# Kernel tuning notes

Measured on AMD Instinct MI355X. Metric: run time of the kernel, lower is better.

Reference implementation:

```python
import jax, jax.numpy as jnp
import numpy as np
from jax import lax

IN_C, OUT_C = 256, 128
HID = (IN_C // 8) // 2   # hidden_channels = 16
NL = 9                   # num_layer
SHIFTS = (1, 5)
DN = ('NCHW', 'OIHW', 'NCHW')

def _base_kernels():
    d1 = np.zeros((4, 1, 3, 3), np.float32)
    d1[0, 0, 0, 0] = -1.0
    d1[1, 0, 0, 1] = -1.0
    d1[2, 0, 0, 2] = -1.0
    d1[3, 0, 1, 2] = -1.0
    d2 = d1[:, :, ::-1, ::-1].copy()
    return np.concatenate([d1, d2], 0)  # (8,1,3,3)

# each of the 8 fixed shift kernels tiled per channel -> (8, HID, 1, 3, 3)
_KER = jnp.asarray(np.tile(_base_kernels()[:, None], (1, HID, 1, 1, 1)))

def _branch(cen, in_w, in_b, w1, w2, w3, sc, shift):
    # input projection conv (kernel 1 or 3, 'same' padding)
    h = lax.conv_general_dilated(cen, in_w, (1, 1), 'SAME', dimension_numbers=DN)
    h = h + in_b[None, :, None, None]
    # 8 fixed dilated depthwise 3x3 convs
    deltas = [lax.conv_general_dilated(h, _KER[k], (1, 1), 'SAME',
                                       rhs_dilation=(shift, shift),
                                       feature_group_count=HID,
                                       dimension_numbers=DN)
              for k in range(8)]
    x = jnp.concatenate(deltas + [h], 1)  # (b, NL*HID, H, W)
    b, c, H, W = x.shape
    xg = x.reshape(b, NL, HID, H, W)
    # grouped 1x1 convs (groups=NL) == per-group 16x16 matmuls
    o1 = jnp.einsum('gdc,bgchw->bgdhw', w1, xg)
    o2 = jnp.einsum('gdc,bgchw->bgdhw', w2, xg)
    o3 = jnp.einsum('gdc,bgchw->bgdhw', w3, xg)
    # logits[b,p,q,h,w] = sc * sum_c o2[b,p,c]*o1[b,q,c]  (torch sums dim=3 of out1*out2*scale)
    logits = sc * jnp.einsum('bpchw,bqchw->bpqhw', o2, o1)
    attn = jax.nn.softmax(logits, axis=2)  # softmax over q (torch dim=2)
    out = jnp.einsum('bpqhw,bqchw->bpchw', attn, o3)
    return out.reshape(b, NL * HID, H, W)

def setup_inputs():
    key = jax.random.key(0)
    ks = jax.random.split(key, 16)
    B, H, W = 4, 192, 192
    s = 0.05
    return {
        'cen': jax.random.normal(ks[0], (B, IN_C, H, W), jnp.float32),
        'in_w0': jax.random.normal(ks[1], (HID, IN_C, 1, 1), jnp.float32) * s,
        'in_b0': jax.random.normal(ks[2], (HID,), jnp.float32) * s,
        'in_w1': jax.random.normal(ks[3], (HID, IN_C, 3, 3), jnp.float32) * s,
        'in_b1': jax.random.normal(ks[4], (HID,), jnp.float32) * s,
        'w1_0': jax.random.normal(ks[5], (NL, HID, HID), jnp.float32) * s,
        'w2_0': jax.random.normal(ks[6], (NL, HID, HID), jnp.float32) * s,
        'w3_0': jax.random.normal(ks[7], (NL, HID, HID), jnp.float32) * s,
        'w1_1': jax.random.normal(ks[8], (NL, HID, HID), jnp.float32) * s,
        'w2_1': jax.random.normal(ks[9], (NL, HID, HID), jnp.float32) * s,
        'w3_1': jax.random.normal(ks[10], (NL, HID, HID), jnp.float32) * s,
        'scale': jax.random.normal(ks[11], (len(SHIFTS),), jnp.float32) * s,
        'out_w': jax.random.normal(ks[12], (OUT_C, NL * HID * len(SHIFTS), 1, 1), jnp.float32) * s,
        'out_b': jax.random.normal(ks[13], (OUT_C,), jnp.float32) * s,
    }

def reference(cen, in_w0, in_b0, in_w1, in_b1, w1_0, w2_0, w3_0,
              w1_1, w2_1, w3_1, scale, out_w, out_b):
    o0 = _branch(cen, in_w0, in_b0, w1_0, w2_0, w3_0, scale[0], SHIFTS[0])
    o1 = _branch(cen, in_w1, in_b1, w1_1, w2_1, w3_1, scale[1], SHIFTS[1])
    cat = jnp.concatenate([o0, o1], 1)  # (b, 288, H, W)
    return jnp.einsum('oi,bihw->bohw', out_w[:, :, 0, 0], cat) + out_b[None, :, None, None]
```

## Files before the change

### kernel.cpp

```cpp
#include <hip/hip_runtime.h>
#include <hip/hip_bf16.h>
#include <cstddef>
#include <cstdint>

#define BATCH 4
#define INC   256
#define HID   16
#define NL    9
#define HH    192
#define WW    192
#define PIX   (HH*WW)
#define BPIX  (BATCH*PIX)
#define OUTC  128
#define CATC  (NL*HID*2)
#define CATK  160

typedef __attribute__((ext_vector_type(8))) short bf16x8;
typedef __attribute__((ext_vector_type(4))) float f32x4;
typedef unsigned short ushort_t;

__device__ inline unsigned short f2bf(float f) {
  unsigned int u = __float_as_uint(f);
  u += 0x7FFF + ((u >> 16) & 1);
  return (unsigned short)(u >> 16);
}
__device__ inline float bf2f(unsigned short s) {
  return __uint_as_float(((unsigned)s) << 16);
}
__device__ inline unsigned pack2(float a, float b) {
  return (unsigned)f2bf(a) | ((unsigned)f2bf(b) << 16);
}
__device__ inline bf16x8 cvt8(float4 a, float4 b) {
  union { bf16x8 v; unsigned u[4]; } r;
  r.u[0] = pack2(a.x, a.y); r.u[1] = pack2(a.z, a.w);
  r.u[2] = pack2(b.x, b.y); r.u[3] = pack2(b.z, b.w);
  return r.v;
}

__global__ __launch_bounds__(256) void kernelP(const float* __restrict__ cen,
                                               ushort_t* __restrict__ th,
                                               ushort_t* __restrict__ tl) {
  __shared__ float t[256][17];
  const int b = blockIdx.z, y = blockIdx.y, x0 = blockIdx.x * 16;
  const int tid = threadIdx.x;
#pragma unroll
  for (int k = 0; k < 16; ++k) {
    int i = tid + k * 256; int c = i >> 4, xl = i & 15;
    t[c][xl] = cen[((size_t)(b * 256 + c)) * PIX + (size_t)y * WW + x0 + xl];
  }
  __syncthreads();
  const size_t obase = (((size_t)b * HH + y) * WW + x0) * 256;
#pragma unroll
  for (int xl = 0; xl < 16; ++xl) {
    float v = t[tid][xl];
    unsigned short hi = f2bf(v);
    th[obase + (size_t)xl * 256 + tid] = hi;
    tl[obase + (size_t)xl * 256 + tid] = f2bf(v - bf2f(hi));
  }
}

__global__ __launch_bounds__(256) void wprepA(
    const float* __restrict__ w0, const float* __restrict__ w1,
    ushort_t* __restrict__ wA0hi, ushort_t* __restrict__ wA0lo,
    ushort_t* __restrict__ wA1hi, ushort_t* __restrict__ wA1lo) {
  int idx = blockIdx.x * 256 + threadIdx.x;
  if (idx < 36864) {
    int j = idx & 7, l = (idx >> 3) & 63, kc = (idx >> 9) & 7, s = idx >> 12;
    int d = l & 15, c = kc * 32 + (l >> 4) * 8 + j;
    float v = w1[(size_t)(d * 256 + c) * 9 + s];
    unsigned short hi = f2bf(v);
    wA1hi[idx] = hi; wA1lo[idx] = f2bf(v - bf2f(hi));
  }
  if (idx < 4096) {
    int j = idx & 7, l = (idx >> 3) & 63, kc = idx >> 9;
    int d = l & 15, c = kc * 32 + (l >> 4) * 8 + j;
    float v = w0[d * 256 + c];
    unsigned short hi = f2bf(v);
    wA0hi[idx] = hi; wA0lo[idx] = f2bf(v - bf2f(hi));
  }
}

__global__ __launch_bounds__(256) void wprepB(const float* __restrict__ out_w,
                                              ushort_t* __restrict__ wb) {
  int idx = blockIdx.x * 256 + threadIdx.x;
  if (idx >= 2 * OUTC * CATK) return;
  int k = idx % CATK; int rest = idx / CATK;
  int o = rest % OUTC; int br = rest / OUTC;
  float v = (k < 144) ? out_w[o * CATC + br * 144 + k] : 0.f;
  wb[idx] = f2bf(v);
}

__global__ __launch_bounds__(256) void wprepM(
    const float* __restrict__ w1_0, const float* __restrict__ w2_0,
    const float* __restrict__ w3_0, const float* __restrict__ w1_1,
    const float* __restrict__ w2_1, const float* __restrict__ w3_1,
    ushort_t* __restrict__ wm) {
  int idx = blockIdx.x * 256 + threadIdx.x;
  if (idx >= 2 * 27 * 512) return;
  int j = idx & 7;
  int lane = (idx >> 3) & 63;
  int blk = idx >> 9;
  int g = blk % 9, mat = (blk / 9) % 3, br = blk / 27;
  int d = lane & 15, k = (lane >> 4) * 8 + j;
  float v = 0.f;
  if (k < 16) {
    const float* w;
    if (br == 0) w = (mat == 0) ? w1_0 : (mat == 1) ? w2_0 : w3_0;
    else         w = (mat == 0) ? w1_1 : (mat == 1) ? w2_1 : w3_1;
    v = w[(g * 16 + d) * 16 + k];
    if (g < 8) v = -v;
  }
  wm[idx] = f2bf(v);
}

template <bool SAFE>
__device__ inline void a_tile(const ushort_t* __restrict__ th,
                              const ushort_t* __restrict__ tl,
                              const ushort_t* __restrict__ wA0hi,
                              const ushort_t* __restrict__ wA0lo,
                              const ushort_t* __restrict__ wA1hi,
                              const ushort_t* __restrict__ wA1lo,
                              int b, int y, int px, f32x4& acc0, f32x4& acc1) {
  const int lane = threadIdx.x & 63;
  const int quad = lane >> 4;
  const bf16x8 bz = {0, 0, 0, 0, 0, 0, 0, 0};
#pragma unroll
  for (int sy = 0; sy < 3; ++sy) {
    const int yy = y + sy - 1;
    const bool yok = SAFE || ((unsigned)yy < (unsigned)HH);
#pragma unroll
    for (int sx = 0; sx < 3; ++sx) {
      const int xx = px + sx - 1;
      const bool ok = SAFE || (yok && ((unsigned)xx < (unsigned)WW));
      const int cy = SAFE ? yy : (ok ? yy : 0);
      const int cx = SAFE ? xx : (ok ? xx : 0);
      const size_t base = (((size_t)(b * HH + cy) * WW) + cx) * 256 + quad * 8;
      const int s = sy * 3 + sx;
      const ushort_t* wh = wA1hi + s * 4096 + lane * 8;
      const ushort_t* wl = wA1lo + s * 4096 + lane * 8;
#pragma unroll
      for (int kc = 0; kc < 8; ++kc) {
        bf16x8 bhi = *(const bf16x8*)(th + base + kc * 32);
        bf16x8 blo = *(const bf16x8*)(tl + base + kc * 32);
        if (!SAFE && !ok) { bhi = bz; blo = bz; }
        bf16x8 ahi = *(const bf16x8*)(wh + kc * 512);
        bf16x8 alo = *(const bf16x8*)(wl + kc * 512);
        acc1 = __builtin_amdgcn_mfma_f32_16x16x32_bf16(ahi, bhi, acc1, 0, 0, 0);
        acc1 = __builtin_amdgcn_mfma_f32_16x16x32_bf16(ahi, blo, acc1, 0, 0, 0);
        acc1 = __builtin_amdgcn_mfma_f32_16x16x32_bf16(alo, bhi, acc1, 0, 0, 0);
        if (s == 4) {
          bf16x8 a0h = *(const bf16x8*)(wA0hi + kc * 512 + lane * 8);
          bf16x8 a0l = *(const bf16x8*)(wA0lo + kc * 512 + lane * 8);
          acc0 = __builtin_amdgcn_mfma_f32_16x16x32_bf16(a0h, bhi, acc0, 0, 0, 0);
          acc0 = __builtin_amdgcn_mfma_f32_16x16x32_bf16(a0h, blo, acc0, 0, 0, 0);
          acc0 = __builtin_amdgcn_mfma_f32_16x16x32_bf16(a0l, bhi, acc0, 0, 0, 0);
        }
      }
    }
  }
}

__global__ __launch_bounds__(256) void kernelA_mfma(
    const ushort_t* __restrict__ th, const ushort_t* __restrict__ tl,
    const ushort_t* __restrict__ wA0hi, const ushort_t* __restrict__ wA0lo,
    const ushort_t* __restrict__ wA1hi, const ushort_t* __restrict__ wA1lo,
    const float* __restrict__ b0, const float* __restrict__ b1,
    float* __restrict__ h0, float* __restrict__ h1) {
  const int lane = threadIdx.x & 63, wave = threadIdx.x >> 6;
  const int n = lane & 15, quad = lane >> 4;
  const int y = blockIdx.y, b = blockIdx.z;
  const int wpx0 = blockIdx.x * 64 + wave * 16;
  const int px = wpx0 + n;
  f32x4 acc0 = {0.f, 0.f, 0.f, 0.f}, acc1 = {0.f, 0.f, 0.f, 0.f};

  const bool safe = (y >= 1) && (y <= HH - 2) && (wpx0 >= 1) && (wpx0 + 16 <= WW - 1);
  if (safe)
    a_tile<true>(th, tl, wA0hi, wA0lo, wA1hi, wA1lo, b, y, px, acc0, acc1);
  else
    a_tile<false>(th, tl, wA0hi, wA0lo, wA1hi, wA1lo, b, y, px, acc0, acc1);

  const size_t pb = ((size_t)b * PIX + (size_t)y * WW + px) * 16 + quad * 4;
  float4 r0, r1;
  r0.x = acc0[0] + b0[quad * 4 + 0]; r0.y = acc0[1] + b0[quad * 4 + 1];
  r0.z = acc0[2] + b0[quad * 4 + 2]; r0.w = acc0[3] + b0[quad * 4 + 3];
  r1.x = acc1[0] + b1[quad * 4 + 0]; r1.y = acc1[1] + b1[quad * 4 + 1];
  r1.z = acc1[2] + b1[quad * 4 + 2]; r1.w = acc1[3] + b1[quad * 4 + 3];
  *(float4*)(h0 + pb) = r0;
  *(float4*)(h1 + pb) = r1;
}

__global__ __launch_bounds__(256) void kernelA_f32(
    const float* __restrict__ cen, const float* __restrict__ w0,
    const float* __restrict__ b0,  const float* __restrict__ w1,
    const float* __restrict__ b1,  float* __restrict__ h0,
    float* __restrict__ h1) {
  __shared__ float lds[16 * 18 * 18];
  const int lx = threadIdx.x, ly = threadIdx.y;
  const int tid = ly * 16 + lx;
  const int x0 = blockIdx.x * 16, y0 = blockIdx.y * 16, b = blockIdx.z;

  float acc0[16], acc1[16];
#pragma unroll
  for (int d = 0; d < 16; ++d) { acc0[d] = 0.f; acc1[d] = 0.f; }

  for (int cb = 0; cb < INC; cb += 16) {
    __syncthreads();
    for (int i = tid; i < 16 * 18 * 18; i += 256) {
      int c = i / 324; int rem = i - c * 324;
      int yy = rem / 18; int xx = rem - yy * 18;
      int gy = y0 + yy - 1, gx = x0 + xx - 1;
      float v = 0.f;
      if (gy >= 0 && gy < HH && gx >= 0 && gx < WW)
        v = cen[(((size_t)b * INC + cb + c) * HH + gy) * WW + gx];
      lds[i] = v;
    }
    __syncthreads();
    for (int c = 0; c < 16; ++c) {
      float v[9];
#pragma unroll
      for (int r = 0; r < 9; ++r) {
        const int dy = r / 3, dx = r - (r / 3) * 3;
        v[r] = lds[(c * 18 + ly + dy) * 18 + lx + dx];
      }
      const int cc = cb + c;
#pragma unroll
      for (int d = 0; d < 16; ++d)
        acc0[d] = fmaf(w0[d * INC + cc], v[4], acc0[d]);
#pragma unroll
      for (int d = 0; d < 16; ++d) {
        float a = acc1[d];
#pragma unroll
        for (int r = 0; r < 9; ++r)
          a = fmaf(w1[(d * INC + cc) * 9 + r], v[r], a);
        acc1[d] = a;
      }
    }
  }
  const int y = y0 + ly, x = x0 + lx;
  const size_t base = ((size_t)b * PIX + (size_t)y * WW + x) * 16;
#pragma unroll
  for (int k = 0; k < 4; ++k) {
    float4 r0, r1;
    r0.x = acc0[4 * k + 0] + b0[4 * k + 0]; r0.y = acc0[4 * k + 1] + b0[4 * k + 1];
    r0.z = acc0[4 * k + 2] + b0[4 * k + 2]; r0.w = acc0[4 * k + 3] + b0[4 * k + 3];
    r1.x = acc1[4 * k + 0] + b1[4 * k + 0]; r1.y = acc1[4 * k + 1] + b1[4 * k + 1];
    r1.z = acc1[4 * k + 2] + b1[4 * k + 2]; r1.w = acc1[4 * k + 3] + b1[4 * k + 3];
    *(float4*)(h0 + base + 4 * k) = r0;
    *(float4*)(h1 + base + 4 * k) = r1;
  }
}

template <int SHIFT, int BRANCH>
__global__ __launch_bounds__(256) void kernelB1m(
    const float* __restrict__ h,
    const ushort_t* __restrict__ wm,
    const float* __restrict__ scale, ushort_t* __restrict__ cat) {
  const int lane = threadIdx.x & 63;
  const int gw = blockIdx.x * 4 + (threadIdx.x >> 6);
  const int bpix0 = gw * 16;
  const int b = bpix0 / PIX;
  const int rem = bpix0 - b * PIX;
  const int y = rem / WW, x0 = rem - y * WW;
  const int n = lane & 15, quad = lane >> 4;
  const float sc = scale[BRANCH];
  const float* __restrict__ hb = h + (size_t)b * PIX * 16;
  const ushort_t* __restrict__ wmb = wm + (size_t)BRANCH * 27 * 512;

  constexpr int DY[9] = {-1, -1, -1, 0, 1, 1, 1, 0, 0};
  constexpr int DX[9] = {-1, 0, 1, 1, 1, 0, -1, -1, 0};

  bf16x8 xf[9];
#pragma unroll
  for (int g = 0; g < 9; ++g) {
    bf16x8 v = {0, 0, 0, 0, 0, 0, 0, 0};
    const int yy = y + DY[g] * SHIFT;
    const int xx = x0 + n + DX[g] * SHIFT;
    if (quad < 2 && (unsigned)yy < (unsigned)HH && (unsigned)xx < (unsigned)WW) {
      const float4* p = (const float4*)(hb + ((size_t)yy * WW + xx) * 16 + quad * 8);
      v = cvt8(p[0], p[1]);
    }
    xf[g] = v;
  }

  const f32x4 zero4 = {0.f, 0.f, 0.f, 0.f};
  f32x4 o1[9], o3[9];
#pragma unroll
  for (int g = 0; g < 9; ++g) {
    const bf16x8 a1 = *(const bf16x8*)(wmb + (0 * 9 + g) * 512 + lane * 8);
    o1[g] = __builtin_amdgcn_mfma_f32_16x16x32_bf16(a1, xf[g], zero4, 0, 0, 0);
  }
#pragma unroll
  for (int g = 0; g < 9; ++g) {
    const bf16x8 a3 = *(const bf16x8*)(wmb + (2 * 9 + g) * 512 + lane * 8);
    o3[g] = __builtin_amdgcn_mfma_f32_16x16x32_bf16(a3, xf[g], zero4, 0, 0, 0);
  }

  ushort_t* __restrict__ crow = cat + (size_t)(bpix0 + n) * CATK;

#pragma unroll
  for (int p = 0; p < 9; ++p) {
    const bf16x8 a2 = *(const bf16x8*)(wmb + (1 * 9 + p) * 512 + lane * 8);
    const f32x4 o2p = __builtin_amdgcn_mfma_f32_16x16x32_bf16(a2, xf[p], zero4, 0, 0, 0);
    float e[9]; float m = -1e30f;
#pragma unroll
    for (int q = 0; q < 9; ++q) {
      float t = (o2p[0] * o1[q][0] + o2p[1] * o1[q][1]) +
                (o2p[2] * o1[q][2] + o2p[3] * o1[q][3]);
      t += __shfl_xor(t, 16);
      t += __shfl_xor(t, 32);
      e[q] = sc * t;
      m = fmaxf(m, e[q]);
    }
    float s = 0.f;
#pragma unroll
    for (int q = 0; q < 9; ++q) { e[q] = __expf(e[q] - m); s += e[q]; }
    const float inv = 1.0f / s;
    f32x4 ov = zero4;
#pragma unroll
    for (int q = 0; q < 9; ++q) {
      const float a = e[q] * inv;
      ov[0] = fmaf(a, o3[q][0], ov[0]);
      ov[1] = fmaf(a, o3[q][1], ov[1]);
      ov[2] = fmaf(a, o3[q][2], ov[2]);
      ov[3] = fmaf(a, o3[q][3], ov[3]);
    }
    uint2 w; w.x = pack2(ov[0], ov[1]); w.y = pack2(ov[2], ov[3]);
    *(uint2*)(crow + p * 16 + quad * 4) = w;
  }
  if (quad < 2)
    *(uint4*)(crow + 144 + quad * 8) = make_uint4(0, 0, 0, 0);
}

template <int BRANCH, bool ACCUM>
__global__ __launch_bounds__(256) void kernelB2(
    const ushort_t* __restrict__ cat, const ushort_t* __restrict__ wb,
    const float* __restrict__ out_b, float* __restrict__ out) {
  const int wave = threadIdx.x >> 6;
  const int lane = threadIdx.x & 63;
  const int tile = blockIdx.x * 4 + wave;
  const int bpix0 = tile * 16;
  const int n = lane & 15, quad = lane >> 4;

  const bf16x8* __restrict__ bp =
      (const bf16x8*)(cat + (size_t)(bpix0 + n) * CATK + quad * 8);
  const ushort_t* __restrict__ wrow0 =
      wb + ((size_t)BRANCH * OUTC + n) * CATK + quad * 8;

  f32x4 acc[8];
#pragma unroll
  for (int mt = 0; mt < 8; ++mt) acc[mt] = (f32x4){0.f, 0.f, 0.f, 0.f};

#pragma unroll
  for (int kc = 0; kc < 5; ++kc) {
    const bf16x8 bfrag = bp[kc * 4];
#pragma unroll
    for (int mt = 0; mt < 8; ++mt) {
      const bf16x8 afrag =
          *(const bf16x8*)(wrow0 + (size_t)mt * 16 * CATK + kc * 32);
      acc[mt] = __builtin_amdgcn_mfma_f32_16x16x32_bf16(afrag, bfrag, acc[mt], 0, 0, 0);
    }
  }

  const int b = bpix0 / PIX;
  const int pin = bpix0 - b * PIX + n;
#pragma unroll
  for (int mt = 0; mt < 8; ++mt) {
#pragma unroll
    for (int i = 0; i < 4; ++i) {
      const int o = mt * 16 + quad * 4 + i;
      const size_t addr = ((size_t)(b * OUTC + o)) * PIX + pin;
      float r = acc[mt][i];
      if (ACCUM) r += out[addr]; else r += out_b[o];
      out[addr] = r;
    }
  }
}

__global__ __launch_bounds__(256) void kernelB2fused(
    const ushort_t* __restrict__ cat0, const ushort_t* __restrict__ cat1,
    const ushort_t* __restrict__ wb, const float* __restrict__ out_b,
    float* __restrict__ out) {
  const int wave = threadIdx.x >> 6;
  const int lane = threadIdx.x & 63;
  const int tile = blockIdx.x * 4 + wave;
  const int bpix0 = tile * 16;
  const int n = lane & 15, quad = lane >> 4;

  f32x4 acc[8];
#pragma unroll
  for (int mt = 0; mt < 8; ++mt) acc[mt] = (f32x4){0.f, 0.f, 0.f, 0.f};

#pragma unroll
  for (int br = 0; br < 2; ++br) {
    const ushort_t* cp = br ? cat1 : cat0;
    const bf16x8* __restrict__ bp =
        (const bf16x8*)(cp + (size_t)(bpix0 + n) * CATK + quad * 8);
    const ushort_t* __restrict__ wrow0 =
        wb + ((size_t)br * OUTC + n) * CATK + quad * 8;
#pragma unroll
    for (int kc = 0; kc < 5; ++kc) {
      const bf16x8 bfrag = bp[kc * 4];
#pragma unroll
      for (int mt = 0; mt < 8; ++mt) {
        const bf16x8 afrag =
            *(const bf16x8*)(wrow0 + (size_t)mt * 16 * CATK + kc * 32);
        acc[mt] = __builtin_amdgcn_mfma_f32_16x16x32_bf16(afrag, bfrag, acc[mt], 0, 0, 0);
      }
    }
  }

  const int b = bpix0 / PIX;
  const int pin = bpix0 - b * PIX + n;
#pragma unroll
  for (int mt = 0; mt < 8; ++mt) {
#pragma unroll
    for (int i = 0; i < 4; ++i) {
      const int o = mt * 16 + quad * 4 + i;
      const size_t addr = ((size_t)(b * OUTC + o)) * PIX + pin;
      out[addr] = acc[mt][i] + out_b[o];
    }
  }
}

extern "C" void kernel_launch(void* const* d_in, const int* in_sizes, int n_in,
                              void* d_out, int out_size, void* d_ws, size_t ws_size,
                              hipStream_t stream) {
  const float* cen   = (const float*)d_in[0];
  const float* in_w0 = (const float*)d_in[1];
  const float* in_b0 = (const float*)d_in[2];
  const float* in_w1 = (const float*)d_in[3];
  const float* in_b1 = (const float*)d_in[4];
  const float* w1_0  = (const float*)d_in[5];
  const float* w2_0  = (const float*)d_in[6];
  const float* w3_0  = (const float*)d_in[7];
  const float* w1_1  = (const float*)d_in[8];
  const float* w2_1  = (const float*)d_in[9];
  const float* w3_1  = (const float*)d_in[10];
  const float* scale = (const float*)d_in[11];
  const float* out_w = (const float*)d_in[12];
  const float* out_b = (const float*)d_in[13];
  float* out = (float*)d_out;

  const size_t H_ELEMS = (size_t)BATCH * HID * PIX;
  const size_t PLANE_E = (size_t)BPIX * 256;
  const size_t CAT_E   = (size_t)BPIX * CATK;

  float* h0 = (float*)d_ws;
  float* h1 = h0 + H_ELEMS;
  ushort_t* wsm = (ushort_t*)(h1 + H_ELEMS);
  ushort_t* wA0hi = wsm;
  ushort_t* wA0lo = wsm + 4096;
  ushort_t* wA1hi = wsm + 8192;
  ushort_t* wA1lo = wsm + 45056;
  ushort_t* wb    = wsm + 81920;
  ushort_t* wm    = wsm + 122880;
  ushort_t* big   = wsm + 150528;

  const size_t base_bytes = 2 * H_ELEMS * 4 + 150528 * 2;
  const size_t fast_need       = base_bytes + 2 * PLANE_E * 2;
  const size_t slow_fused_need = base_bytes + 2 * CAT_E * 2;
  const bool fast  = ws_size >= fast_need;
  const bool fused = fast || ws_size >= slow_fused_need;

  ushort_t* cat0 = big;
  ushort_t* cat1 = fused ? (big + CAT_E) : big;

  hipLaunchKernelGGL(wprepB, dim3((2 * OUTC * CATK + 255) / 256), dim3(256), 0,
                     stream, out_w, wb);
  hipLaunchKernelGGL(wprepM, dim3((2 * 27 * 512 + 255) / 256), dim3(256), 0,
                     stream, w1_0, w2_0, w3_0, w1_1, w2_1, w3_1, wm);

  if (fast) {
    ushort_t* th = big;
    ushort_t* tl = big + PLANE_E;
    hipLaunchKernelGGL(wprepA, dim3(144), dim3(256), 0, stream,
                       in_w0, in_w1, wA0hi, wA0lo, wA1hi, wA1lo);
    hipLaunchKernelGGL(kernelP, dim3(WW / 16, HH, BATCH), dim3(256), 0, stream,
                       cen, th, tl);
    hipLaunchKernelGGL(kernelA_mfma, dim3(3, HH, BATCH), dim3(256), 0, stream,
                       th, tl, wA0hi, wA0lo, wA1hi, wA1lo, in_b0, in_b1, h0, h1);
  } else {
    hipLaunchKernelGGL(kernelA_f32, dim3(WW / 16, HH / 16, BATCH), dim3(16, 16), 0,
                       stream, cen, in_w0, in_b0, in_w1, in_b1, h0, h1);
  }

  const int nb1 = (BPIX / 16) / 4;
  const int nb2 = (BPIX / 16) / 4;

  if (fused) {
    hipLaunchKernelGGL((kernelB1m<1, 0>), dim3(nb1), dim3(256), 0, stream,
                       h0, wm, scale, cat0);
    hipLaunchKernelGGL((kernelB1m<5, 1>), dim3(nb1), dim3(256), 0, stream,
                       h1, wm, scale, cat1);
    hipLaunchKernelGGL(kernelB2fused, dim3(nb2), dim3(256), 0, stream,
                       cat0, cat1, wb, out_b, out);
  } else {
    hipLaunchKernelGGL((kernelB1m<1, 0>), dim3(nb1), dim3(256), 0, stream,
                       h0, wm, scale, cat0);
    hipLaunchKernelGGL((kernelB2<0, false>), dim3(nb2), dim3(256), 0, stream,
                       cat0, wb, out_b, out);
    hipLaunchKernelGGL((kernelB1m<5, 1>), dim3(nb1), dim3(256), 0, stream,
                       h1, w1_1 ? wm : wm, scale, cat1);
    hipLaunchKernelGGL((kernelB2<1, true>), dim3(nb2), dim3(256), 0, stream,
                       cat1, wb, out_b, out);
  }
}
```

Before: 659.0 us.

## Reorder bf16 input planes by channel chunk and remap blocks across XCDs

Stores the split bf16 hi/lo input planes as [b][y][kc][x][32] instead of pixel-major 256-channel rows, so each MFMA operand load for a 32-channel chunk reads contiguous data across neighbouring pixels. kernelA_mfma now uses a 1D grid, and both kernelA_mfma and kernelB1m remap block indices so that contiguous tiles go to the same XCD (an index/8 plus index%8 swizzle), aiming to improve L2 locality for the overlapping stencil reads. The swizzle hardcodes a 2304-block stride, which matches the grid sizes here but ties correctness to these shapes.

```diff
diff --git a/kernel.cpp b/kernel.cpp
--- a/kernel.cpp
+++ b/kernel.cpp
@@ -15,6 +15,9 @@
 #define CATC  (NL*HID*2)
 #define CATK  160
 
+#define KCSTRIDE (WW*32)
+#define ROWSTRIDE (8*WW*32)
+
 typedef __attribute__((ext_vector_type(8))) short bf16x8;
 typedef __attribute__((ext_vector_type(4))) float f32x4;
 typedef unsigned short ushort_t;
@@ -49,13 +52,17 @@
     t[c][xl] = cen[((size_t)(b * 256 + c)) * PIX + (size_t)y * WW + x0 + xl];
   }
   __syncthreads();
-  const size_t obase = (((size_t)b * HH + y) * WW + x0) * 256;
+  const size_t rowbase = (size_t)(b * HH + y) * ROWSTRIDE;
+  const int kcq = tid >> 5;
+  const int c32 = tid & 31;
+  const size_t obase = rowbase + (size_t)kcq * KCSTRIDE + c32;
 #pragma unroll
   for (int xl = 0; xl < 16; ++xl) {
     float v = t[tid][xl];
     unsigned short hi = f2bf(v);
-    th[obase + (size_t)xl * 256 + tid] = hi;
-    tl[obase + (size_t)xl * 256 + tid] = f2bf(v - bf2f(hi));
+    const size_t a = obase + (size_t)(x0 + xl) * 32;
+    th[a] = hi;
+    tl[a] = f2bf(v - bf2f(hi));
   }
 }
 
@@ -134,14 +141,15 @@
       const bool ok = SAFE || (yok && ((unsigned)xx < (unsigned)WW));
       const int cy = SAFE ? yy : (ok ? yy : 0);
       const int cx = SAFE ? xx : (ok ? xx : 0);
-      const size_t base = (((size_t)(b * HH + cy) * WW) + cx) * 256 + quad * 8;
+      const size_t base =
+          (size_t)(b * HH + cy) * ROWSTRIDE + (size_t)cx * 32 + quad * 8;
       const int s = sy * 3 + sx;
       const ushort_t* wh = wA1hi + s * 4096 + lane * 8;
       const ushort_t* wl = wA1lo + s * 4096 + lane * 8;
 #pragma unroll
       for (int kc = 0; kc < 8; ++kc) {
-        bf16x8 bhi = *(const bf16x8*)(th + base + kc * 32);
-        bf16x8 blo = *(const bf16x8*)(tl + base + kc * 32);
+        bf16x8 bhi = *(const bf16x8*)(th + base + kc * KCSTRIDE);
+        bf16x8 blo = *(const bf16x8*)(tl + base + kc * KCSTRIDE);
         if (!SAFE && !ok) { bhi = bz; blo = bz; }
         bf16x8 ahi = *(const bf16x8*)(wh + kc * 512);
         bf16x8 alo = *(const bf16x8*)(wl + kc * 512);
@@ -166,10 +174,14 @@
     const ushort_t* __restrict__ wA1hi, const ushort_t* __restrict__ wA1lo,
     const float* __restrict__ b0, const float* __restrict__ b1,
     float* __restrict__ h0, float* __restrict__ h1) {
+  const int lt = (blockIdx.x & 7) * (2304 / 8) + (blockIdx.x >> 3);
+  const int xb = lt % 3;
+  const int y  = (lt / 3) % HH;
+  const int b  = lt / (3 * HH);
+
   const int lane = threadIdx.x & 63, wave = threadIdx.x >> 6;
   const int n = lane & 15, quad = lane >> 4;
-  const int y = blockIdx.y, b = blockIdx.z;
-  const int wpx0 = blockIdx.x * 64 + wave * 16;
+  const int wpx0 = xb * 64 + wave * 16;
   const int px = wpx0 + n;
   f32x4 acc0 = {0.f, 0.f, 0.f, 0.f}, acc1 = {0.f, 0.f, 0.f, 0.f};
 
@@ -256,7 +268,8 @@
     const ushort_t* __restrict__ wm,
     const float* __restrict__ scale, ushort_t* __restrict__ cat) {
   const int lane = threadIdx.x & 63;
-  const int gw = blockIdx.x * 4 + (threadIdx.x >> 6);
+  const int bw = (blockIdx.x & 7) * (2304 / 8) + (blockIdx.x >> 3);
+  const int gw = bw * 4 + (threadIdx.x >> 6);
   const int bpix0 = gw * 16;
   const int b = bpix0 / PIX;
   const int rem = bpix0 - b * PIX;
@@ -477,7 +490,7 @@
                        in_w0, in_w1, wA0hi, wA0lo, wA1hi, wA1lo);
     hipLaunchKernelGGL(kernelP, dim3(WW / 16, HH, BATCH), dim3(256), 0, stream,
                        cen, th, tl);
-    hipLaunchKernelGGL(kernelA_mfma, dim3(3, HH, BATCH), dim3(256), 0, stream,
+    hipLaunchKernelGGL(kernelA_mfma, dim3(3 * HH * BATCH), dim3(256), 0, stream,
                        th, tl, wA0hi, wA0lo, wA1hi, wA1lo, in_b0, in_b1, h0, h1);
   } else {
     hipLaunchKernelGGL(kernelA_f32, dim3(WW / 16, HH / 16, BATCH), dim3(16, 16), 0,
```

Measured after the change: 653.3 us. About the same (-0.9%).
